# Performance work log

Hardware: AMD Instinct MI355X
Metric: run time of the kernel (lower is better)

## Reference

```python
import jax, jax.numpy as jnp
import numpy as np

B, T, C = 2, 2048, 1024
H = 16
D = C // H  # head_dim = 64


def setup_inputs() -> dict:
    key = jax.random.key(0)
    k1, k2, k3, k4, k5 = jax.random.split(key, 5)
    s = 0.02
    return {
        "x": jax.random.normal(k1, (B, T, C), dtype=jnp.float32),
        "w_qkv": jax.random.normal(k2, (C, 3 * C), dtype=jnp.float32) * s,
        "b_qkv": jnp.zeros((3 * C,), dtype=jnp.float32),
        "w_proj": jax.random.normal(k3, (C, C), dtype=jnp.float32) * s,
        "b_proj": jnp.zeros((C,), dtype=jnp.float32),
    }


def reference(x, w_qkv, b_qkv, w_proj, b_proj):
    b, t, c = x.shape
    qkv = x @ w_qkv + b_qkv                      # [B,T,3C]
    q, k, v = jnp.split(qkv, 3, axis=-1)
    # [B,T,C] -> [B,H,T,D]
    q = q.reshape(b, t, H, D).transpose(0, 2, 1, 3)
    k = k.reshape(b, t, H, D).transpose(0, 2, 1, 3)
    v = v.reshape(b, t, H, D).transpose(0, 2, 1, 3)
    att = jnp.einsum("bhqd,bhkd->bhqk", q, k) / jnp.sqrt(jnp.float32(D))
    causal = jnp.tril(jnp.ones((t, t), dtype=bool))  # True where allowed
    att = jnp.where(causal, att, -jnp.inf)
    att = jax.nn.softmax(att, axis=-1)
    out = jnp.einsum("bhqk,bhkd->bhqd", att, v)      # [B,H,T,D]
    out = out.transpose(0, 2, 1, 3).reshape(b, t, c)
    return out @ w_proj + b_proj
```

## Files before the change

### kernel.cpp

```cpp
#include <hip/hip_runtime.h>
#include <hip/hip_bf16.h>
#include <math.h>
#include <stdint.h>

#define B_ 2
#define T_ 2048
#define C_ 1024
#define H_ 16
#define D_ 64

typedef __attribute__((ext_vector_type(8))) short bf16x8;
typedef __attribute__((ext_vector_type(4))) float f32x4;

__device__ inline short f2bf(float f) {
  __hip_bfloat16 h = __float2bfloat16(f);
  return *(short*)&h;
}

__device__ inline void async16(const void* g, void* l) {
  __builtin_amdgcn_global_load_lds(
      (const __attribute__((address_space(1))) uint32_t*)g,
      (__attribute__((address_space(3))) uint32_t*)l, 16, 0, 0);
}


__global__ __launch_bounds__(256) void prep(
    const float* __restrict__ X, const float* __restrict__ Wq,
    const float* __restrict__ Wp, short* __restrict__ Xb,
    short* __restrict__ Wqt, short* __restrict__ Wpt) {
  const int tid = threadIdx.x;
  const int blk = blockIdx.x;
  __shared__ short Ts[64][68];

  if (blk < 512) {
    int t = blk * 256 + tid;
    int m = t >> 5, g = t & 31;
    const float* src = X + (size_t)m * C_ + g * 32;
    short* dst = Xb + (size_t)m * C_ + g * 32;
    int xv = (m >> 1) & 3;
    short out[32];
#pragma unroll
    for (int ch = 0; ch < 4; ++ch) {
      int sc = ch ^ xv;
#pragma unroll
      for (int e = 0; e < 8; e += 4) {
        float4 v = *(const float4*)(src + sc * 8 + e);
        out[ch * 8 + e + 0] = f2bf(v.x);
        out[ch * 8 + e + 1] = f2bf(v.y);
        out[ch * 8 + e + 2] = f2bf(v.z);
        out[ch * 8 + e + 3] = f2bf(v.w);
      }
    }
#pragma unroll
    for (int q = 0; q < 4; ++q) *(uint4*)(dst + q * 8) = *(uint4*)(out + q * 8);
    return;
  }

  const float* W;
  short* Wt;
  int N, n0, k0;
  if (blk < 1280) {
    int i = blk - 512;
    W = Wq; Wt = Wqt; N = 3 * C_;
    n0 = (i % 48) * 64; k0 = (i / 48) * 64;
  } else {
    int i = blk - 1280;
    W = Wp; Wt = Wpt; N = C_;
    n0 = (i & 15) * 64; k0 = (i >> 4) * 64;
  }
  {
    int r = tid >> 2, c0 = (tid & 3) * 16;
    const float* src = W + (size_t)(k0 + r) * N + n0 + c0;
#pragma unroll
    for (int u = 0; u < 16; u += 4) {
      float4 v = *(const float4*)(src + u);
      Ts[r][c0 + u + 0] = f2bf(v.x);
      Ts[r][c0 + u + 1] = f2bf(v.y);
      Ts[r][c0 + u + 2] = f2bf(v.z);
      Ts[r][c0 + u + 3] = f2bf(v.w);
    }
  }
  __syncthreads();
#pragma unroll
  for (int p = 0; p < 2; ++p) {
    int n = (tid >> 3) + p * 32;
    int kc = tid & 7;
    int xv = ((n0 + n) >> 1) & 3;
    int ka = kc * 8;
    int dk = (ka & ~31) | ((((ka >> 3) & 3) ^ xv) << 3);
    short tmp[8];
#pragma unroll
    for (int u = 0; u < 8; ++u) tmp[u] = Ts[ka + u][n];
    *(uint4*)(Wt + (size_t)(n0 + n) * 1024 + k0 + dk) = *(uint4*)tmp;
  }
}

template <int N, int BN, bool QKV>
__global__ __launch_bounds__(256) void gemm_mfma(
    const short* __restrict__ A, const short* __restrict__ Bt,
    const float* __restrict__ bias, short* __restrict__ Qp,
    short* __restrict__ Kp, short* __restrict__ Vp, float* __restrict__ Cout) {
  constexpr int NJ = BN / 32;
  const int tid = threadIdx.x;
  const int wave = tid >> 6, lane = tid & 63;
  const int quad = lane >> 4, l16 = lane & 15;
  const int wm = wave >> 1, wn = wave & 1;
  const int m0 = blockIdx.y * 128, n0 = blockIdx.x * BN;

  __shared__ short As[2][4096];
  __shared__ short Bs[2][BN * 32];

  const int srow = tid >> 2, skc = tid & 3;
  const size_t arow0 = (size_t)(m0 + srow) * 1024 + skc * 8;
  const size_t brow0 = (size_t)(n0 + srow) * 1024 + skc * 8;

  f32x4 acc[4][NJ] = {};

  const int xi = quad ^ ((l16 >> 1) & 3);
  int aoff[4], boff[NJ];
#pragma unroll
  for (int i = 0; i < 4; ++i) aoff[i] = (wm * 64 + i * 16 + l16) * 32 + xi * 8;
#pragma unroll
  for (int j = 0; j < NJ; ++j)
    boff[j] = (wn * (BN / 2) + j * 16 + l16) * 32 + xi * 8;

  auto stage = [&](int k0, int buf) {
    async16(A + arow0 + k0, &As[buf][tid * 8]);
    async16(A + arow0 + (size_t)64 * 1024 + k0, &As[buf][2048 + tid * 8]);
    async16(Bt + brow0 + k0, &Bs[buf][tid * 8]);
    if (BN == 128)
      async16(Bt + brow0 + (size_t)64 * 1024 + k0, &Bs[buf][2048 + tid * 8]);
  };

  stage(0, 0);
  for (int kt = 0; kt < 32; ++kt) {
    const int buf = kt & 1;
    __syncthreads();
    if (kt < 31) stage((kt + 1) * 32, buf ^ 1);

    bf16x8 af[4], bfr[NJ];
#pragma unroll
    for (int i = 0; i < 4; ++i) af[i] = *(const bf16x8*)&As[buf][aoff[i]];
#pragma unroll
    for (int j = 0; j < NJ; ++j) bfr[j] = *(const bf16x8*)&Bs[buf][boff[j]];
#pragma unroll
    for (int i = 0; i < 4; ++i)
#pragma unroll
      for (int j = 0; j < NJ; ++j)
        acc[i][j] = __builtin_amdgcn_mfma_f32_16x16x32_bf16(af[i], bfr[j],
                                                            acc[i][j], 0, 0, 0);
  }

  float bj[NJ];
#pragma unroll
  for (int j = 0; j < NJ; ++j) bj[j] = bias[n0 + wn * (BN / 2) + j * 16 + l16];

  if (QKV) {
#pragma unroll
    for (int i = 0; i < 4; ++i) {
#pragma unroll
      for (int reg = 0; reg < 4; ++reg) {
        int m = m0 + wm * 64 + i * 16 + quad * 4 + reg;
        int b = m >> 11, t = m & (T_ - 1);
#pragma unroll
        for (int j = 0; j < NJ; ++j) {
          int n = n0 + wn * (BN / 2) + j * 16 + l16;
          float v = acc[i][j][reg] + bj[j];
          int sel = n >> 10, cc = n & (C_ - 1);
          int hh = cc >> 6, d = cc & 63;
          size_t base = (size_t)(b * H_ + hh) * 131072 + (size_t)(t >> 6) * 4096;
          if (sel == 0) {
            Qp[base + (d >> 3) * 512 + (t & 63) * 8 + (d & 7)] = f2bf(v * 0.125f);
          } else if (sel == 1) {
            Kp[base + (d >> 3) * 512 + (t & 63) * 8 + (d & 7)] = f2bf(v);
          } else {
            Vp[base + ((t & 63) >> 3) * 512 + d * 8 + (t & 7)] = f2bf(v);
          }
        }
      }
    }
  } else {
#pragma unroll
    for (int i = 0; i < 4; ++i) {
#pragma unroll
      for (int reg = 0; reg < 4; ++reg) {
        int m = m0 + wm * 64 + i * 16 + quad * 4 + reg;
#pragma unroll
        for (int j = 0; j < NJ; ++j) {
          int n = n0 + wn * (BN / 2) + j * 16 + l16;
          Cout[(size_t)m * N + n] = acc[i][j][reg] + bj[j];
        }
      }
    }
  }
}

__global__ __launch_bounds__(256, 4) void attn_kernel(
    const short* __restrict__ Qt, const short* __restrict__ Kt,
    const short* __restrict__ Vt, short* __restrict__ attb) {
  const int tid = threadIdx.x;
  const int wave = tid >> 6, lane = tid & 63;
  const int quad = lane >> 4, l16 = lane & 15;

  const int blk = blockIdx.x;
  const int bh = (blk >> 5) & 31;
  const int k2 = blk >> 8;
  int qtt = ((blk & 31) + 8 * (k2 >> 1)) & 31;
  const int qt = (k2 & 1) ? (31 - qtt) : qtt;
  const int h = bh & 15, b = bh >> 4;
  const int q0 = qt * 64;

  const short* Qg = Qt + (size_t)bh * 131072;
  const short* Kg = Kt + (size_t)bh * 131072;
  const short* Vg = Vt + (size_t)bh * 131072;

  __shared__ short Ks[2][4096];
  __shared__ short Vs[2][4096];
  __shared__ short Ps[4096];

  const int rowl = 16 * wave + l16;

  bf16x8 bq[2];
#pragma unroll
  for (int f = 0; f < 2; ++f)
    bq[f] = *(const bf16x8*)(Qg + (size_t)(qt * 8 + 4 * f + quad) * 512 +
                             rowl * 8);

  async16(Kg + tid * 8, &Ks[0][tid * 8]);
  async16(Kg + 2048 + tid * 8, &Ks[0][2048 + tid * 8]);
  async16(Vg + tid * 8, &Vs[0][tid * 8]);
  async16(Vg + 2048 + tid * 8, &Vs[0][2048 + tid * 8]);

  f32x4 oacc[4] = {};
  float lsum = 0.f;

  for (int kt = 0; kt <= qt; ++kt) {
    const int buf = kt & 1;
    __syncthreads();
    if (kt < qt) {
      const short* kp = Kg + (size_t)(kt + 1) * 4096;
      const short* vp = Vg + (size_t)(kt + 1) * 4096;
      async16(kp + tid * 8, &Ks[buf ^ 1][tid * 8]);
      async16(kp + 2048 + tid * 8, &Ks[buf ^ 1][2048 + tid * 8]);
      async16(vp + tid * 8, &Vs[buf ^ 1][tid * 8]);
      async16(vp + 2048 + tid * 8, &Vs[buf ^ 1][2048 + tid * 8]);
    }

    f32x4 sacc[4] = {};
#pragma unroll
    for (int c = 0; c < 4; ++c) {
#pragma unroll
      for (int f = 0; f < 2; ++f) {
        bf16x8 ak = *(const bf16x8*)&Ks[buf][((4 * f + quad) * 64 + 16 * c + l16) * 8];
        sacc[c] = __builtin_amdgcn_mfma_f32_16x16x32_bf16(ak, bq[f], sacc[c], 0, 0, 0);
      }
    }

    const bool diag = (kt == qt);
#pragma unroll
    for (int c = 0; c < 4; ++c) {
      short4 pk;
#pragma unroll
      for (int reg = 0; reg < 4; ++reg) {
        int keyl = 16 * c + 4 * quad + reg;
        float p = (diag && keyl > rowl) ? 0.f : __expf(sacc[c][reg]);
        lsum += p;
        ((short*)&pk)[reg] = f2bf(p);
      }
      *(short4*)&Ps[(2 * c + (quad >> 1)) * 512 + rowl * 8 + (quad & 1) * 4] = pk;
    }

    __asm__ volatile("s_waitcnt lgkmcnt(0)" ::: "memory");

    bf16x8 ap[2];
#pragma unroll
    for (int f = 0; f < 2; ++f)
      ap[f] = *(const bf16x8*)&Ps[(4 * f + quad) * 512 + rowl * 8];
#pragma unroll
    for (int n = 0; n < 4; ++n) {
#pragma unroll
      for (int f = 0; f < 2; ++f) {
        bf16x8 bv = *(const bf16x8*)&Vs[buf][((4 * f + quad) * 64 + 16 * n + l16) * 8];
        oacc[n] = __builtin_amdgcn_mfma_f32_16x16x32_bf16(ap[f], bv, oacc[n], 0, 0, 0);
      }
    }
  }

  lsum += __shfl_xor(lsum, 16);
  lsum += __shfl_xor(lsum, 32);
  float linv[4];
#pragma unroll
  for (int reg = 0; reg < 4; ++reg)
    linv[reg] = 1.0f / __shfl(lsum, 4 * quad + reg, 64);

#pragma unroll
  for (int reg = 0; reg < 4; ++reg) {
    const int row = q0 + 16 * wave + 4 * quad + reg;
    const int m = b * T_ + row;
    const int xv = (m >> 1) & 3;
#pragma unroll
    for (int n = 0; n < 4; ++n) {
      int c = h * 64 + 16 * n + l16;
      int cs = (c & ~31) | ((((c >> 3) & 3) ^ xv) << 3) | (c & 7);
      attb[(size_t)m * C_ + cs] = f2bf(oacc[n][reg] * linv[reg]);
    }
  }
}

extern "C" void kernel_launch(void* const* d_in, const int* in_sizes, int n_in,
                              void* d_out, int out_size, void* d_ws, size_t ws_size,
                              hipStream_t stream) {
  const float* x      = (const float*)d_in[0];
  const float* w_qkv  = (const float*)d_in[1];
  const float* b_qkv  = (const float*)d_in[2];
  const float* w_proj = (const float*)d_in[3];
  const float* b_proj = (const float*)d_in[4];
  float* out = (float*)d_out;

  const size_t per = (size_t)B_ * H_ * T_ * D_;
  short* Qp   = (short*)d_ws;
  short* Kp   = Qp + per;
  short* Vp   = Kp + per;
  short* attb = Vp + per;
  short* xb   = attb + per;
  short* wqt  = xb + per;
  short* wpt  = wqt + (size_t)3 * C_ * C_;

  prep<<<1536, 256, 0, stream>>>(x, w_qkv, w_proj, xb, wqt, wpt);

  gemm_mfma<3 * C_, 128, true><<<dim3(24, 32), 256, 0, stream>>>(
      xb, wqt, b_qkv, Qp, Kp, Vp, nullptr);

  attn_kernel<<<dim3(1024), 256, 0, stream>>>(Qp, Kp, Vp, attb);

  gemm_mfma<C_, 64, false><<<dim3(16, 32), 256, 0, stream>>>(
      attb, wpt, b_proj, nullptr, nullptr, nullptr, out);
}
```

Measured before the change: 189.9 us.

## Replace double-buffered K32 GEMM pipeline with single-buffer K64 tiles

The GEMM mainloop no longer double-buffers 32-wide K tiles with prefetch. Instead it loads a 64-wide K tile into a single LDS buffer, synchronizes, and then issues two MFMA k-steps per iteration. This halves the number of loop iterations and barriers. The cost is that global-to-LDS loads no longer overlap with compute, and the LDS row stride changes from 32 to 64, which interacts with the existing swizzle pattern.

```diff
diff --git a/kernel.cpp b/kernel.cpp
--- a/kernel.cpp
+++ b/kernel.cpp
@@ -101,54 +101,61 @@
     const float* __restrict__ bias, short* __restrict__ Qp,
     short* __restrict__ Kp, short* __restrict__ Vp, float* __restrict__ Cout) {
   constexpr int NJ = BN / 32;
+  constexpr int BP = BN / 32;
   const int tid = threadIdx.x;
   const int wave = tid >> 6, lane = tid & 63;
   const int quad = lane >> 4, l16 = lane & 15;
   const int wm = wave >> 1, wn = wave & 1;
   const int m0 = blockIdx.y * 128, n0 = blockIdx.x * BN;
 
-  __shared__ short As[2][4096];
-  __shared__ short Bs[2][BN * 32];
-
-  const int srow = tid >> 2, skc = tid & 3;
-  const size_t arow0 = (size_t)(m0 + srow) * 1024 + skc * 8;
-  const size_t brow0 = (size_t)(n0 + srow) * 1024 + skc * 8;
+  __shared__ short As[128 * 64];
+  __shared__ short Bs[BN * 64];
+
+  size_t ab[4], bb[BP];
+#pragma unroll
+  for (int p = 0; p < 4; ++p)
+    ab[p] = (size_t)(m0 + p * 32 + (tid >> 3)) * 1024 + (tid & 7) * 8;
+#pragma unroll
+  for (int p = 0; p < BP; ++p)
+    bb[p] = (size_t)(n0 + p * 32 + (tid >> 3)) * 1024 + (tid & 7) * 8;
 
   f32x4 acc[4][NJ] = {};
 
   const int xi = quad ^ ((l16 >> 1) & 3);
   int aoff[4], boff[NJ];
 #pragma unroll
-  for (int i = 0; i < 4; ++i) aoff[i] = (wm * 64 + i * 16 + l16) * 32 + xi * 8;
+  for (int i = 0; i < 4; ++i) aoff[i] = (wm * 64 + i * 16 + l16) * 64 + xi * 8;
 #pragma unroll
   for (int j = 0; j < NJ; ++j)
-    boff[j] = (wn * (BN / 2) + j * 16 + l16) * 32 + xi * 8;
-
-  auto stage = [&](int k0, int buf) {
-    async16(A + arow0 + k0, &As[buf][tid * 8]);
-    async16(A + arow0 + (size_t)64 * 1024 + k0, &As[buf][2048 + tid * 8]);
-    async16(Bt + brow0 + k0, &Bs[buf][tid * 8]);
-    if (BN == 128)
-      async16(Bt + brow0 + (size_t)64 * 1024 + k0, &Bs[buf][2048 + tid * 8]);
-  };
-
-  stage(0, 0);
-  for (int kt = 0; kt < 32; ++kt) {
-    const int buf = kt & 1;
+    boff[j] = (wn * (BN / 2) + j * 16 + l16) * 64 + xi * 8;
+
+  for (int k0 = 0; k0 < 1024; k0 += 64) {
     __syncthreads();
-    if (kt < 31) stage((kt + 1) * 32, buf ^ 1);
-
-    bf16x8 af[4], bfr[NJ];
-#pragma unroll
-    for (int i = 0; i < 4; ++i) af[i] = *(const bf16x8*)&As[buf][aoff[i]];
-#pragma unroll
-    for (int j = 0; j < NJ; ++j) bfr[j] = *(const bf16x8*)&Bs[buf][boff[j]];
-#pragma unroll
-    for (int i = 0; i < 4; ++i)
-#pragma unroll
-      for (int j = 0; j < NJ; ++j)
-        acc[i][j] = __builtin_amdgcn_mfma_f32_16x16x32_bf16(af[i], bfr[j],
-                                                            acc[i][j], 0, 0, 0);
+#pragma unroll
+    for (int p = 0; p < 4; ++p) async16(A + ab[p] + k0, As + (p * 256 + tid) * 8);
+#pragma unroll
+    for (int p = 0; p < BP; ++p) async16(Bt + bb[p] + k0, Bs + (p * 256 + tid) * 8);
+    __syncthreads();
+
+    bf16x8 af[4][2], bfr[NJ][2];
+#pragma unroll
+    for (int i = 0; i < 4; ++i) {
+      af[i][0] = *(const bf16x8*)(As + aoff[i]);
+      af[i][1] = *(const bf16x8*)(As + aoff[i] + 32);
+    }
+#pragma unroll
+    for (int j = 0; j < NJ; ++j) {
+      bfr[j][0] = *(const bf16x8*)(Bs + boff[j]);
+      bfr[j][1] = *(const bf16x8*)(Bs + boff[j] + 32);
+    }
+#pragma unroll
+    for (int f = 0; f < 2; ++f)
+#pragma unroll
+      for (int i = 0; i < 4; ++i)
+#pragma unroll
+        for (int j = 0; j < NJ; ++j)
+          acc[i][j] = __builtin_amdgcn_mfma_f32_16x16x32_bf16(
+              af[i][f], bfr[j][f], acc[i][j], 0, 0, 0);
   }
 
   float bj[NJ];
```

New measurement: 190.9 us. About the same (+0.6%).

## Split-K output projection with atomics, single-buffered LDS in GEMM

Applied to the files above, without the earlier changes.

Adds a K-split template parameter to the GEMM. The output projection now uses BN=128 tiles split across two K halves and accumulated with atomic adds into a zeroed output, which needs an extra memset. The double-buffered LDS prefetch is replaced with a single buffer that loads and then syncs each step. That removes the overlap of global loads with MFMA work for both GEMMs, but lowers LDS use and may raise occupancy.

```diff
diff --git a/kernel.cpp b/kernel.cpp
--- a/kernel.cpp
+++ b/kernel.cpp
@@ -95,20 +95,22 @@
   }
 }
 
-template <int N, int BN, bool QKV>
+template <int N, int BN, bool QKV, int KSPLIT>
 __global__ __launch_bounds__(256) void gemm_mfma(
     const short* __restrict__ A, const short* __restrict__ Bt,
     const float* __restrict__ bias, short* __restrict__ Qp,
     short* __restrict__ Kp, short* __restrict__ Vp, float* __restrict__ Cout) {
   constexpr int NJ = BN / 32;
+  constexpr int KL = 1024 / KSPLIT;
   const int tid = threadIdx.x;
   const int wave = tid >> 6, lane = tid & 63;
   const int quad = lane >> 4, l16 = lane & 15;
   const int wm = wave >> 1, wn = wave & 1;
   const int m0 = blockIdx.y * 128, n0 = blockIdx.x * BN;
-
-  __shared__ short As[2][4096];
-  __shared__ short Bs[2][BN * 32];
+  const int kbase = blockIdx.z * KL;
+
+  __shared__ short As[128 * 32];
+  __shared__ short Bs[BN * 32];
 
   const int srow = tid >> 2, skc = tid & 3;
   const size_t arow0 = (size_t)(m0 + srow) * 1024 + skc * 8;
@@ -124,25 +126,20 @@
   for (int j = 0; j < NJ; ++j)
     boff[j] = (wn * (BN / 2) + j * 16 + l16) * 32 + xi * 8;
 
-  auto stage = [&](int k0, int buf) {
-    async16(A + arow0 + k0, &As[buf][tid * 8]);
-    async16(A + arow0 + (size_t)64 * 1024 + k0, &As[buf][2048 + tid * 8]);
-    async16(Bt + brow0 + k0, &Bs[buf][tid * 8]);
+  for (int k0 = kbase; k0 < kbase + KL; k0 += 32) {
+    __syncthreads();
+    async16(A + arow0 + k0, As + tid * 8);
+    async16(A + arow0 + (size_t)64 * 1024 + k0, As + 2048 + tid * 8);
+    async16(Bt + brow0 + k0, Bs + tid * 8);
     if (BN == 128)
-      async16(Bt + brow0 + (size_t)64 * 1024 + k0, &Bs[buf][2048 + tid * 8]);
-  };
-
-  stage(0, 0);
-  for (int kt = 0; kt < 32; ++kt) {
-    const int buf = kt & 1;
+      async16(Bt + brow0 + (size_t)64 * 1024 + k0, Bs + 2048 + tid * 8);
     __syncthreads();
-    if (kt < 31) stage((kt + 1) * 32, buf ^ 1);
 
     bf16x8 af[4], bfr[NJ];
 #pragma unroll
-    for (int i = 0; i < 4; ++i) af[i] = *(const bf16x8*)&As[buf][aoff[i]];
-#pragma unroll
-    for (int j = 0; j < NJ; ++j) bfr[j] = *(const bf16x8*)&Bs[buf][boff[j]];
+    for (int i = 0; i < 4; ++i) af[i] = *(const bf16x8*)(As + aoff[i]);
+#pragma unroll
+    for (int j = 0; j < NJ; ++j) bfr[j] = *(const bf16x8*)(Bs + boff[j]);
 #pragma unroll
     for (int i = 0; i < 4; ++i)
 #pragma unroll
@@ -153,7 +150,10 @@
 
   float bj[NJ];
 #pragma unroll
-  for (int j = 0; j < NJ; ++j) bj[j] = bias[n0 + wn * (BN / 2) + j * 16 + l16];
+  for (int j = 0; j < NJ; ++j) {
+    float bv = bias[n0 + wn * (BN / 2) + j * 16 + l16];
+    bj[j] = (KSPLIT > 1 && blockIdx.z != 0) ? 0.f : bv;
+  }
 
   if (QKV) {
 #pragma unroll
@@ -188,7 +188,12 @@
 #pragma unroll
         for (int j = 0; j < NJ; ++j) {
           int n = n0 + wn * (BN / 2) + j * 16 + l16;
-          Cout[(size_t)m * N + n] = acc[i][j][reg] + bj[j];
+          float v = acc[i][j][reg] + bj[j];
+          if (KSPLIT > 1) {
+            unsafeAtomicAdd(&Cout[(size_t)m * N + n], v);
+          } else {
+            Cout[(size_t)m * N + n] = v;
+          }
         }
       }
     }
@@ -326,13 +331,15 @@
   short* wqt  = xb + per;
   short* wpt  = wqt + (size_t)3 * C_ * C_;
 
+  hipMemsetAsync(out, 0, (size_t)out_size * sizeof(float), stream);
+
   prep<<<1536, 256, 0, stream>>>(x, w_qkv, w_proj, xb, wqt, wpt);
 
-  gemm_mfma<3 * C_, 128, true><<<dim3(24, 32), 256, 0, stream>>>(
+  gemm_mfma<3 * C_, 128, true, 1><<<dim3(24, 32, 1), 256, 0, stream>>>(
       xb, wqt, b_qkv, Qp, Kp, Vp, nullptr);
 
   attn_kernel<<<dim3(1024), 256, 0, stream>>>(Qp, Kp, Vp, attb);
 
-  gemm_mfma<C_, 64, false><<<dim3(16, 32), 256, 0, stream>>>(
+  gemm_mfma<C_, 128, false, 2><<<dim3(8, 32, 2), 256, 0, stream>>>(
       attb, wpt, b_proj, nullptr, nullptr, nullptr, out);
 }
```

Result: slower. 202.1 us (+6.5%).
